# Optimization experiments

Measured on AMD Instinct MI355X. Metric: run time of the kernel, lower is better.

## Reference

```python
import jax, jax.numpy as jnp
import numpy as np

M, N = 64, 8192
IN_DIM, HID, OUT = 6, 256, 128


def _mlp3(x, params):
    # three Linear+ReLU layers
    for W, b in params:
        x = jax.nn.relu(x @ W + b)
    return x


def setup_inputs() -> dict:
    key = jax.random.key(0)
    ks = jax.random.split(key, 16)
    def lin(k, fan_in, fan_out):
        bound = 1.0 / np.sqrt(fan_in)
        kw, kb = jax.random.split(k)
        W = jax.random.uniform(kw, (fan_in, fan_out), jnp.float32, -bound, bound)
        b = jax.random.uniform(kb, (fan_out,), jnp.float32, -bound, bound)
        return W, b
    feat = jax.random.normal(ks[0], (M, N, IN_DIM), jnp.float32)
    eW1, eb1 = lin(ks[1], IN_DIM, HID)
    eW2, eb2 = lin(ks[2], HID, HID)
    eW3, eb3 = lin(ks[3], HID, HID)
    sW1, sb1 = lin(ks[4], HID, OUT)
    sW2, sb2 = lin(ks[5], OUT, OUT)
    sW3, sb3 = lin(ks[6], OUT, OUT)
    cW, cb = lin(ks[7], IN_DIM + HID + OUT, 1)
    return {
        'feat': feat,
        'eW1': eW1, 'eb1': eb1, 'eW2': eW2, 'eb2': eb2, 'eW3': eW3, 'eb3': eb3,
        'sW1': sW1, 'sb1': sb1, 'sW2': sW2, 'sb2': sb2, 'sW3': sW3, 'sb3': sb3,
        'cW': cW, 'cb': cb,
    }


def reference(feat, eW1, eb1, eW2, eb2, eW3, eb3,
              sW1, sb1, sW2, sb2, sW3, sb3, cW, cb):
    # embed MLP over all points: [M, N, HID]
    hidden = _mlp3(feat, [(eW1, eb1), (eW2, eb2), (eW3, eb3)])
    # max-pool over points within each bbox: [M, HID]
    pooled = jnp.max(hidden, axis=1)
    # segment MLP on pooled feature: [M, OUT]
    seg = _mlp3(pooled, [(sW1, sb1), (sW2, sb2), (sW3, sb3)])
    # concat [feat, hidden, seg broadcast over points]: [M, N, 6+HID+OUT]
    seg_tiled = jnp.broadcast_to(seg[:, None, :], (feat.shape[0], feat.shape[1], seg.shape[-1]))
    concat = jnp.concatenate([feat, hidden, seg_tiled], axis=-1)
    # classifier -> score [M, N]
    score = (concat @ cW)[..., 0] + cb[0]
    # per-bbox min/max rescale to [-1, 1]
    smin = jnp.min(score, axis=1, keepdims=True)
    smax = jnp.max(score, axis=1, keepdims=True)
    score = (score - smin) / (smax - smin) * 2.0 - 1.0
    return score
```

## Files before the change

### kernel.cpp

```cpp
#include <hip/hip_runtime.h>


typedef __attribute__((ext_vector_type(8))) short short8;
typedef __attribute__((ext_vector_type(4))) float f32x4;
typedef __attribute__((ext_vector_type(4))) unsigned int u32x4;

#define THREADS 512

__device__ __forceinline__ unsigned short f2bf(float f) {
  union { float f; unsigned int u; } x; x.f = f;
  unsigned int r = x.u + 0x7fffu + ((x.u >> 16) & 1u);
  return (unsigned short)(r >> 16);
}

__device__ __forceinline__ unsigned int cvt_pk_bf16(float lo, float hi) {
  unsigned int r;
  asm("v_cvt_pk_bf16_f32 %0, %1, %2" : "=v"(r) : "v"(lo), "v"(hi));
  return r;
}

__global__ void pn_pack(const float* __restrict__ W1,
                        const float* __restrict__ W2,
                        const float* __restrict__ W3,
                        unsigned short* __restrict__ wp) {
  int e = blockIdx.x * 256 + threadIdx.x;
  const float* src; int Kreal, base, r;
  if (e < 8192)       { src = W1; Kreal = 6;   base = 0;     r = e; }
  else if (e < 73728) { src = W2; Kreal = 256; base = 8192;  r = e - 8192; }
  else                { src = W3; Kreal = 256; base = 73728; r = e - 73728; }
  int j   = r & 7;
  int col = (r >> 3) & 15;
  int hi  = (r >> 7) & 3;
  int ct  = (r >> 9) & 15;
  int s   = r >> 13;
  int k = s * 32 + hi * 8 + j;
  int c = ct * 16 + col;
  float v = (k < Kreal) ? src[k * 256 + c] : 0.0f;
  wp[base + r] = f2bf(v);
}

__device__ __forceinline__ int hswz(int byteoff) {
  return byteoff ^ (((byteoff >> 7) & 7) << 4);
}

__device__ __forceinline__ void gemm256p(const unsigned short* __restrict__ wpL,
                                         const unsigned short* hP,
                                         int cgrp, int pgrp, int lane,
                                         int l15, int hi,
                                         f32x4 (&acc)[4][4]) {
#pragma unroll
  for (int ks = 0; ks < 8; ++ks) {
    short8 afr[4], bfr[4];
#pragma unroll
    for (int cf = 0; cf < 4; ++cf)
      afr[cf] = *(const short8*)(wpL +
                 (((((ks * 16 + cgrp * 4 + cf) * 4) + hi) * 16 + l15) << 3));
#pragma unroll
    for (int pf = 0; pf < 4; ++pf) {
      int byteoff = ((ks * 8 + (pgrp * 4 + pf)) * 64 + lane) * 16;
      bfr[pf] = *(const short8*)((const char*)hP + hswz(byteoff));
    }
#pragma unroll
    for (int cf = 0; cf < 4; ++cf)
#pragma unroll
      for (int pf = 0; pf < 4; ++pf)
        acc[cf][pf] = __builtin_amdgcn_mfma_f32_16x16x32_bf16(
            afr[cf], bfr[pf], acc[cf][pf], 0, 0, 0);
  }
}

__device__ __forceinline__ void acc_init(f32x4 (&acc)[4][4], const float* bv,
                                         int cgrp, int hi) {
#pragma unroll
  for (int cf = 0; cf < 4; ++cf) {
    f32x4 bi = *(const f32x4*)(bv + cgrp * 64 + cf * 16 + hi * 4);
#pragma unroll
    for (int pf = 0; pf < 4; ++pf) acc[cf][pf] = bi;
  }
}

__device__ __forceinline__ void epi_hp(f32x4 (&acc)[4][4], unsigned short* hP,
                                       int cgrp, int pgrp, int l15, int hi) {
#pragma unroll
  for (int cf = 0; cf < 4; ++cf) {
    int ks2 = cgrp * 2 + (cf >> 1);
    int chi = (cf & 1) * 2 + (hi >> 1);
    int j0  = (hi & 1) * 4;
#pragma unroll
    for (int pf = 0; pf < 4; ++pf) {
      f32x4 a = acc[cf][pf];
      unsigned int lo  = cvt_pk_bf16(fmaxf(a[0], 0.0f), fmaxf(a[1], 0.0f));
      unsigned int hi2 = cvt_pk_bf16(fmaxf(a[2], 0.0f), fmaxf(a[3], 0.0f));
      unsigned long long w = (unsigned long long)lo | ((unsigned long long)hi2 << 32);
      int byteoff = (((ks2 * 8 + (pgrp * 4 + pf)) * 64 + chi * 16 + l15) * 16)
                  + j0 * 2;
      *(unsigned long long*)((char*)hP + hswz(byteoff)) = w;
    }
  }
}

__global__ __launch_bounds__(THREADS, 1) void pn_main(
    const float* __restrict__ feat,
    const unsigned short* __restrict__ wp,
    const float* __restrict__ b1,
    const float* __restrict__ b2,
    const float* __restrict__ b3,
    const float* __restrict__ cW,
    float* __restrict__ out) {
  __shared__ unsigned short hP[64 * 1024 / 2];
  __shared__ unsigned short hF[128 * 8];
  __shared__ float biasL[3 * 256];
  __shared__ float whL[256];
  float* sPart = (float*)hF;

  const int tid  = threadIdx.x;
  const int lane = tid & 63;
  const int wave = tid >> 6;
  const int l15  = lane & 15;
  const int hi   = lane >> 4;
  const int cgrp = wave & 3;
  const int pgrp = wave >> 2;

  const int blk = blockIdx.x;
  const int m   = blk >> 6;
  const int n0  = (blk & 63) << 7;
  const int g0  = m * 8192 + n0;

  if (tid < 256) {
    biasL[tid]       = b1[tid];
    biasL[256 + tid] = b2[tid];
    biasL[512 + tid] = b3[tid];
    whL[tid]         = cW[6 + tid];
  }

  float fdot = 0.0f;
  if (tid < 128) {
    const float* fp = feat + (size_t)(g0 + tid) * 6;
    float f0 = fp[0], f1 = fp[1], f2 = fp[2], f3 = fp[3], f4 = fp[4], f5 = fp[5];
    fdot = f0 * cW[0] + f1 * cW[1] + f2 * cW[2] + f3 * cW[3] + f4 * cW[4] + f5 * cW[5];
    u32x4 v;
    v[0] = cvt_pk_bf16(f0, f1);
    v[1] = cvt_pk_bf16(f2, f3);
    v[2] = cvt_pk_bf16(f4, f5);
    v[3] = 0;
    *(u32x4*)(hF + tid * 8) = v;
  }
  __syncthreads();

  f32x4 acc[4][4];
  const short8 zero8 = {0, 0, 0, 0, 0, 0, 0, 0};

  acc_init(acc, biasL + 0, cgrp, hi);
  {
    short8 afr[4], bfr[4];
#pragma unroll
    for (int cf = 0; cf < 4; ++cf)
      afr[cf] = *(const short8*)(wp + ((((cgrp * 4 + cf) * 4 + hi) * 16 + l15) << 3));
#pragma unroll
    for (int pf = 0; pf < 4; ++pf) {
      int p = pgrp * 64 + pf * 16 + l15;
      bfr[pf] = (hi == 0) ? *(const short8*)(hF + p * 8) : zero8;
    }
#pragma unroll
    for (int cf = 0; cf < 4; ++cf)
#pragma unroll
      for (int pf = 0; pf < 4; ++pf)
        acc[cf][pf] = __builtin_amdgcn_mfma_f32_16x16x32_bf16(
            afr[cf], bfr[pf], acc[cf][pf], 0, 0, 0);
  }
  epi_hp(acc, hP, cgrp, pgrp, l15, hi);
  __syncthreads();

  acc_init(acc, biasL + 256, cgrp, hi);
  gemm256p(wp + 8192, hP, cgrp, pgrp, lane, l15, hi, acc);
  __syncthreads();
  epi_hp(acc, hP, cgrp, pgrp, l15, hi);
  __syncthreads();

  acc_init(acc, biasL + 512, cgrp, hi);
  gemm256p(wp + 73728, hP, cgrp, pgrp, lane, l15, hi, acc);

  float part[4] = {0.f, 0.f, 0.f, 0.f};
#pragma unroll
  for (int cf = 0; cf < 4; ++cf) {
    int c0 = cgrp * 64 + cf * 16 + hi * 4;
#pragma unroll
    for (int r = 0; r < 4; ++r) {
      float wv = whL[c0 + r];
#pragma unroll
      for (int pf = 0; pf < 4; ++pf)
        part[pf] += fmaxf(acc[cf][pf][r], 0.0f) * wv;
    }
  }
#pragma unroll
  for (int off = 16; off < 64; off <<= 1)
#pragma unroll
    for (int pf = 0; pf < 4; ++pf)
      part[pf] += __shfl_xor(part[pf], off);
  if (hi == 0) {
#pragma unroll
    for (int pf = 0; pf < 4; ++pf)
      sPart[cgrp * 128 + pgrp * 64 + pf * 16 + l15] = part[pf];
  }
  __syncthreads();

  if (tid < 128) {
    float s = sPart[tid] + sPart[128 + tid] + sPart[256 + tid] + sPart[384 + tid]
            + fdot;
    out[g0 + tid] = s;
  }
}

__global__ void pn_finalize(float* __restrict__ out) {
  __shared__ float smn[4], smx[4];
  int mrow = blockIdx.x;
  float* row = out + mrow * 8192;
  float v[32];
  float mn = 1e30f, mx = -1e30f;
#pragma unroll
  for (int i = 0; i < 32; ++i) {
    v[i] = row[threadIdx.x + i * 256];
    mn = fminf(mn, v[i]);
    mx = fmaxf(mx, v[i]);
  }
#pragma unroll
  for (int off = 1; off < 64; off <<= 1) {
    mn = fminf(mn, __shfl_xor(mn, off));
    mx = fmaxf(mx, __shfl_xor(mx, off));
  }
  int w = threadIdx.x >> 6;
  if ((threadIdx.x & 63) == 0) { smn[w] = mn; smx[w] = mx; }
  __syncthreads();
  mn = fminf(fminf(smn[0], smn[1]), fminf(smn[2], smn[3]));
  mx = fmaxf(fmaxf(smx[0], smx[1]), fmaxf(smx[2], smx[3]));
  float sc = 2.0f / (mx - mn);
#pragma unroll
  for (int i = 0; i < 32; ++i)
    row[threadIdx.x + i * 256] = (v[i] - mn) * sc - 1.0f;
}

extern "C" void kernel_launch(void* const* d_in, const int* in_sizes, int n_in,
                              void* d_out, int out_size, void* d_ws, size_t ws_size,
                              hipStream_t stream) {
  const float* feat = (const float*)d_in[0];
  const float* eW1  = (const float*)d_in[1];
  const float* eb1  = (const float*)d_in[2];
  const float* eW2  = (const float*)d_in[3];
  const float* eb2  = (const float*)d_in[4];
  const float* eW3  = (const float*)d_in[5];
  const float* eb3  = (const float*)d_in[6];
  const float* cW   = (const float*)d_in[13];
  float* out = (float*)d_out;
  unsigned short* wpack = (unsigned short*)d_ws;

  pn_pack<<<544, 256, 0, stream>>>(eW1, eW2, eW3, wpack);
  pn_main<<<4096, THREADS, 0, stream>>>(feat, wpack, eb1, eb2, eb3, cW, out);
  pn_finalize<<<64, 256, 0, stream>>>(out);
}
```

Baseline: 146.0 us.

## Stage GEMM weights into double-buffered LDS via async global-to-LDS loads

Layers 2 and 3 previously read weight fragments straight from global memory on every k-step. They now stream 16 KB weight slices into two LDS buffers with global_load_lds, prefetching two slices ahead. A single 16-iteration loop with explicit barriers and waitcnts covers both layers, and the layer-2 epilogue is folded in at iteration 7. The XOR swizzle on the activation buffer is dropped, and the first-layer weights are loaded into registers early. The aim is to hide global/L2 latency behind MFMA work, at the cost of extra LDS, two barriers per k-step, and possible bank conflicts from the unswizzled layout.

```diff
diff --git a/kernel.cpp b/kernel.cpp
--- a/kernel.cpp
+++ b/kernel.cpp
@@ -6,6 +6,9 @@
 typedef __attribute__((ext_vector_type(4))) unsigned int u32x4;
 
 #define THREADS 512
+
+#define LDS_AS(p) ((__attribute__((address_space(3))) unsigned int*)(p))
+#define GLB_AS(p) ((const __attribute__((address_space(1))) unsigned int*)(p))
 
 __device__ __forceinline__ unsigned short f2bf(float f) {
   union { float f; unsigned int u; } x; x.f = f;
@@ -39,33 +42,16 @@
   wp[base + r] = f2bf(v);
 }
 
-__device__ __forceinline__ int hswz(int byteoff) {
-  return byteoff ^ (((byteoff >> 7) & 7) << 4);
-}
-
-__device__ __forceinline__ void gemm256p(const unsigned short* __restrict__ wpL,
-                                         const unsigned short* hP,
-                                         int cgrp, int pgrp, int lane,
-                                         int l15, int hi,
-                                         f32x4 (&acc)[4][4]) {
-#pragma unroll
-  for (int ks = 0; ks < 8; ++ks) {
-    short8 afr[4], bfr[4];
-#pragma unroll
-    for (int cf = 0; cf < 4; ++cf)
-      afr[cf] = *(const short8*)(wpL +
-                 (((((ks * 16 + cgrp * 4 + cf) * 4) + hi) * 16 + l15) << 3));
-#pragma unroll
-    for (int pf = 0; pf < 4; ++pf) {
-      int byteoff = ((ks * 8 + (pgrp * 4 + pf)) * 64 + lane) * 16;
-      bfr[pf] = *(const short8*)((const char*)hP + hswz(byteoff));
-    }
-#pragma unroll
-    for (int cf = 0; cf < 4; ++cf)
-#pragma unroll
-      for (int pf = 0; pf < 4; ++pf)
-        acc[cf][pf] = __builtin_amdgcn_mfma_f32_16x16x32_bf16(
-            afr[cf], bfr[pf], acc[cf][pf], 0, 0, 0);
+
+__device__ __forceinline__ void stage16k(const unsigned short* __restrict__ gsrc,
+                                         unsigned short* lbase,
+                                         int wave, int lane) {
+#pragma unroll
+  for (int r = 0; r < 2; ++r) {
+    int row = r * 8 + wave;
+    const unsigned short* g = gsrc + row * 512 + lane * 8;
+    unsigned short* l = lbase + row * 512;
+    __builtin_amdgcn_global_load_lds(GLB_AS(g), LDS_AS(l), 16, 0, 0);
   }
 }
 
@@ -92,9 +78,8 @@
       unsigned int lo  = cvt_pk_bf16(fmaxf(a[0], 0.0f), fmaxf(a[1], 0.0f));
       unsigned int hi2 = cvt_pk_bf16(fmaxf(a[2], 0.0f), fmaxf(a[3], 0.0f));
       unsigned long long w = (unsigned long long)lo | ((unsigned long long)hi2 << 32);
-      int byteoff = (((ks2 * 8 + (pgrp * 4 + pf)) * 64 + chi * 16 + l15) * 16)
-                  + j0 * 2;
-      *(unsigned long long*)((char*)hP + hswz(byteoff)) = w;
+      int us = ((ks2 * 8 + pgrp * 4 + pf) * 64 + chi * 16 + l15) * 8 + j0;
+      *(unsigned long long*)(hP + us) = w;
     }
   }
 }
@@ -107,7 +92,8 @@
     const float* __restrict__ b3,
     const float* __restrict__ cW,
     float* __restrict__ out) {
-  __shared__ unsigned short hP[64 * 1024 / 2];
+  __shared__ unsigned short hP[8 * 8 * 512];
+  __shared__ unsigned short wst[2][16 * 512];
   __shared__ unsigned short hF[128 * 8];
   __shared__ float biasL[3 * 256];
   __shared__ float whL[256];
@@ -125,6 +111,9 @@
   const int m   = blk >> 6;
   const int n0  = (blk & 63) << 7;
   const int g0  = m * 8192 + n0;
+
+  stage16k(wp + 8192, wst[0], wave, lane);
+  stage16k(wp + 8192 + 8192, wst[1], wave, lane);
 
   if (tid < 256) {
     biasL[tid]       = b1[tid];
@@ -145,40 +134,76 @@
     v[3] = 0;
     *(u32x4*)(hF + tid * 8) = v;
   }
+
+  short8 w1r[4];
+#pragma unroll
+  for (int cf = 0; cf < 4; ++cf)
+    w1r[cf] = *(const short8*)(wp + ((((cgrp * 4 + cf) * 4 + hi) * 16 + l15) << 3));
+
   __syncthreads();
 
   f32x4 acc[4][4];
   const short8 zero8 = {0, 0, 0, 0, 0, 0, 0, 0};
 
   acc_init(acc, biasL + 0, cgrp, hi);
-  {
+#pragma unroll
+  for (int pf = 0; pf < 4; ++pf) {
+    int p = pgrp * 64 + pf * 16 + l15;
+    short8 b = (hi == 0) ? *(const short8*)(hF + p * 8) : zero8;
+#pragma unroll
+    for (int cf = 0; cf < 4; ++cf)
+      acc[cf][pf] = __builtin_amdgcn_mfma_f32_16x16x32_bf16(
+          w1r[cf], b, acc[cf][pf], 0, 0, 0);
+  }
+  epi_hp(acc, hP, cgrp, pgrp, l15, hi);
+  acc_init(acc, biasL + 256, cgrp, hi);
+  __syncthreads();
+
+#pragma unroll 1
+  for (int t = 0; t < 16; ++t) {
+    const unsigned short* wt = wst[t & 1];
+    int ksl = t & 7;
     short8 afr[4], bfr[4];
 #pragma unroll
     for (int cf = 0; cf < 4; ++cf)
-      afr[cf] = *(const short8*)(wp + ((((cgrp * 4 + cf) * 4 + hi) * 16 + l15) << 3));
-#pragma unroll
-    for (int pf = 0; pf < 4; ++pf) {
-      int p = pgrp * 64 + pf * 16 + l15;
-      bfr[pf] = (hi == 0) ? *(const short8*)(hF + p * 8) : zero8;
-    }
+      afr[cf] = *(const short8*)(wt + (((cgrp * 4 + cf) * 64 + lane) << 3));
+#pragma unroll
+    for (int pf = 0; pf < 4; ++pf)
+      bfr[pf] = *(const short8*)(hP + (((ksl * 8 + pgrp * 4 + pf) * 64 + lane) << 3));
 #pragma unroll
     for (int cf = 0; cf < 4; ++cf)
 #pragma unroll
       for (int pf = 0; pf < 4; ++pf)
         acc[cf][pf] = __builtin_amdgcn_mfma_f32_16x16x32_bf16(
             afr[cf], bfr[pf], acc[cf][pf], 0, 0, 0);
-  }
-  epi_hp(acc, hP, cgrp, pgrp, l15, hi);
-  __syncthreads();
-
-  acc_init(acc, biasL + 256, cgrp, hi);
-  gemm256p(wp + 8192, hP, cgrp, pgrp, lane, l15, hi, acc);
-  __syncthreads();
-  epi_hp(acc, hP, cgrp, pgrp, l15, hi);
-  __syncthreads();
-
-  acc_init(acc, biasL + 512, cgrp, hi);
-  gemm256p(wp + 73728, hP, cgrp, pgrp, lane, l15, hi, acc);
+
+    if (t == 7) {
+      __builtin_amdgcn_sched_barrier(0);
+      __builtin_amdgcn_s_barrier();
+      __builtin_amdgcn_sched_barrier(0);
+      stage16k(wp + 73728 + 8192, wst[1], wave, lane);
+      epi_hp(acc, hP, cgrp, pgrp, l15, hi);
+      acc_init(acc, biasL + 512, cgrp, hi);
+      asm volatile("s_waitcnt vmcnt(2) lgkmcnt(0)" ::: "memory");
+      __builtin_amdgcn_sched_barrier(0);
+      __builtin_amdgcn_s_barrier();
+    } else {
+      __builtin_amdgcn_sched_barrier(0);
+      __builtin_amdgcn_s_barrier();
+      __builtin_amdgcn_sched_barrier(0);
+      if (t + 2 < 16) {
+        int s = t + 2;
+        const unsigned short* src = (s < 8) ? (wp + 8192 + s * 8192)
+                                            : (wp + 73728 + (s - 8) * 8192);
+        stage16k(src, wst[t & 1], wave, lane);
+        asm volatile("s_waitcnt vmcnt(2)" ::: "memory");
+      } else {
+        asm volatile("s_waitcnt vmcnt(0)" ::: "memory");
+      }
+      __builtin_amdgcn_sched_barrier(0);
+      __builtin_amdgcn_s_barrier();
+    }
+  }
 
   float part[4] = {0.f, 0.f, 0.f, 0.f};
 #pragma unroll
```

Measured after the change: 209.4 us. 43.4% more time.
